# Kernel tuning notes

Measured on AMD Instinct MI355X. Metric: run time of the kernel, lower is better.

The kernel has to match this reference:

```python
import jax, jax.numpy as jnp
import numpy as np

N = 2048      # atoms in one graph
C = 8         # energy_num_channels
CONV = 332.07156


def setup_inputs() -> dict:
    key = jax.random.key(0)
    ks = jax.random.split(key, 12)
    X = jax.random.normal(ks[0], (N, 3), dtype=jnp.float32) * 10.0   # coords (Angstrom-ish)
    embs = jax.random.normal(ks[1], (N, C), dtype=jnp.float32)        # GNN atom embeddings
    qs = jax.random.normal(ks[2], (N,), dtype=jnp.float32) * 0.5      # partial charges
    Ps = jnp.zeros((N, 3), dtype=jnp.float32)                          # dipoles (zeros, as in EnergyNet.forward)
    w0 = jax.random.uniform(ks[3], (N,), dtype=jnp.float32) * 0.5 + 0.1  # vdw_dep
    s0 = jax.random.uniform(ks[4], (N,), dtype=jnp.float32) + 1.0        # vdw_sig
    chainidx = jax.random.randint(ks[5], (N,), 0, 2)
    sf_elec = jax.random.normal(ks[6], (2 * C + 1, 1), dtype=jnp.float32) * 0.1
    sf_elec = sf_elec.at[-1, 0].set(1.0)
    born_factor = jax.random.normal(ks[7], (C,), dtype=jnp.float32) * 0.1 + 1.0
    die_factor = jax.random.normal(ks[8], (C,), dtype=jnp.float32) * 0.1 + 4.0
    depth_factor = jax.random.normal(ks[9], (2 * C, 1), dtype=jnp.float32) * 0.05 + 1.0
    radius_factor = jax.random.normal(ks[10], (2 * C, 1), dtype=jnp.float32) * 0.05 + 1.0
    return dict(X=X, embs=embs, qs=qs, Ps=Ps, w0=w0, s0=s0, chainidx=chainidx,
                sf_elec=sf_elec, born_factor=born_factor, die_factor=die_factor,
                depth_factor=depth_factor, radius_factor=radius_factor)


def _nan_guard(e):
    return jnp.where(jnp.isnan(e), jnp.asarray(1e-6, e.dtype), e)


def _energies(X, embs, qs, Ps, w0, s0, mask, sf_elec, born, die, depth, radius):
    # shared pairwise geometry (original recomputes this in each submodule)
    V = X[None, :, :] - X[:, None, :]               # V[i,j] = X[j]-X[i], [N,N,3]
    D = jnp.sqrt(jnp.sum(V * V + 1e-6, axis=-1))    # [N,N]
    Vp = V + 1e-6
    Vn = Vp / jnp.maximum(jnp.linalg.norm(Vp, axis=-1, keepdims=True), 1e-12)
    invD = 1.0 / (D + 1e-6)

    # ---- Electrostatics ----
    f = sf_elec[:, 0]
    # screening = emb_j . f[:C] + emb_i . f[C:2C] + invD * f[2C]  (decomposed matmul)
    sf = (embs @ f[:C])[None, :] + (embs @ f[C:2 * C])[:, None] + invD * f[2 * C]
    OqP = jnp.einsum('ijk,ik->ij', Vn, Ps)
    OPP = Ps @ Ps.T
    Q12 = jnp.outer(qs, qs)
    invD3 = invD * invD * invD
    E_qq = Q12 * invD * sf
    E_qP = OqP * invD * invD3
    E_PP = OPP * invD3 * invD3
    E_elec = 0.5 * jnp.sum(CONV * mask * (E_qq + E_qP + E_PP))
    E_elec = _nan_guard(E_elec)

    # ---- Solvation (calc_pair=False => only Born self term) ----
    atomic_die = embs @ die + 1e-6
    R = embs @ born + 1.0
    E_self = -(1.0 - 1.0 / atomic_die) * qs / (R + 1e-6)
    E_solv = CONV * jnp.sum(E_self) * 0.01
    E_solv = _nan_guard(E_solv)

    # ---- vdW ----
    rf = radius[:, 0]
    df = depth[:, 0]
    sig_r = jax.nn.sigmoid((embs @ rf[:C])[None, :] + (embs @ rf[C:])[:, None])
    # NB: original broadcasting makes s0_ij = 2*s0[j] (column-only), reproduced faithfully
    s = (2.0 * s0)[None, :] * (0.8 * sig_r + 0.4)
    repl = 5.0 * jnp.exp(-0.3 * D * D * D) * mask
    Dm = D - s
    attr = (jnp.exp(-(Dm - 0.3) ** 2) + jnp.exp(-3.0 * Dm * Dm)
            + jnp.exp(-10.0 * Dm * Dm)) / 3.0 * mask
    w0j = jnp.sqrt(w0 * w0 + 1e-6)[None, :]        # original w0_ij also column-only
    sig_d = jax.nn.sigmoid((embs @ df[:C])[None, :] + (embs @ df[C:])[:, None])
    w = w0j * (sig_d + 0.5)
    E_vdw = jnp.sum(-w * attr + repl)
    E_vdw = _nan_guard(E_vdw)

    return E_vdw, E_elec, E_solv


def reference(X, embs, qs, Ps, w0, s0, chainidx, sf_elec, born_factor, die_factor,
              depth_factor, radius_factor):
    mask = (chainidx[None, :] != chainidx[:, None]).astype(X.dtype)
    return _energies(X, embs, qs, Ps, w0, s0, mask,
                     sf_elec, born_factor, die_factor, depth_factor, radius_factor)
```

## Files before the change

### kernel.cpp

```cpp
#include <hip/hip_runtime.h>

#define NA 2048
#define CDIM 8
#define CONVF 332.07156f
#define PTI 8
#define PTHREADS 512
#define CH 1024
#define PAIR_GRID 258


__global__ __launch_bounds__(256) void pre_kernel(
    const float* __restrict__ X,
    const float* __restrict__ embs,
    const float* __restrict__ qs,
    const float* __restrict__ Ps,
    const float* __restrict__ w0,
    const float* __restrict__ s0,
    const int* __restrict__ chain,
    const float* __restrict__ sf_elec,
    const float* __restrict__ born,
    const float* __restrict__ die,
    const float* __restrict__ depth,
    const float* __restrict__ radius,
    int* __restrict__ wsi,
    float* __restrict__ wsf,
    float4* __restrict__ g0, float4* __restrict__ g1,
    float4* __restrict__ g2, float4* __restrict__ g3,
    float* __restrict__ d_out)
{
    const int b = blockIdx.x, t = threadIdx.x;
    if (b == 8) {
        if (t < 2) d_out[t] = 0.0f;
        return;
    }
    const int i = b * 256 + t;

    const int4 f0 = ((const int4*)chain)[2 * t];
    const int4 f1 = ((const int4*)chain)[2 * t + 1];
    const int s = (f0.x == 0) + (f0.y == 0) + (f0.z == 0) + (f0.w == 0) +
                  (f1.x == 0) + (f1.y == 0) + (f1.z == 0) + (f1.w == 0);
    const int lane = t & 63, wv = t >> 6;
    int x = s;
#pragma unroll
    for (int off = 1; off < 64; off <<= 1) {
        int y = __shfl_up(x, off);
        if (lane >= off) x += y;
    }
    __shared__ int wtot[4];
    __shared__ int gpre[256];
    __shared__ float fsum[4];
    if (lane == 63) wtot[wv] = x;
    __syncthreads();
    int wbase = 0, tot = 0;
#pragma unroll
    for (int k = 0; k < 4; ++k) {
        int v = wtot[k];
        if (k < wv) wbase += v;
        tot += v;
    }
    gpre[t] = wbase + x - s;
    __syncthreads();

    const int g = i >> 3;
    int base = gpre[g];
    for (int a = (g << 3); a < i; ++a) base += (chain[a] == 0);
    const int flag = (chain[i] == 0);
    const int slot = flag ? base : tot + (i - base);

    float e[CDIM];
#pragma unroll
    for (int k = 0; k < CDIM; ++k) e[k] = embs[i * CDIM + k];
    float sfA = 0.f, sfB = 0.f, rfA = 0.f, rfB = 0.f, dfA = 0.f, dfB = 0.f;
    float dieV = 0.f, Rv = 0.f;
#pragma unroll
    for (int k = 0; k < CDIM; ++k) {
        sfA  += e[k] * sf_elec[k];
        sfB  += e[k] * sf_elec[CDIM + k];
        rfA  += e[k] * radius[k];
        rfB  += e[k] * radius[CDIM + k];
        dfA  += e[k] * depth[k];
        dfB  += e[k] * depth[CDIM + k];
        dieV += e[k] * die[k];
        Rv   += e[k] * born[k];
    }
    dieV += 1e-6f;
    Rv += 1.0f;
    const float q = qs[i];
    float es = -(1.0f - 1.0f / dieV) * q / (Rv + 1e-6f);

    const float erA = __expf(-rfA), edA = __expf(-dfA);
    const float erB = __expf(-rfB), edB = __expf(-dfB);
    const float w0j = sqrtf(w0[i] * w0[i] + 1e-6f);

    g0[slot] = make_float4(X[i * 3 + 0], X[i * 3 + 1], X[i * 3 + 2], q);
    g1[slot] = make_float4(sfA, erA, edA, w0j);
    g2[slot] = make_float4(2.0f * s0[i], Ps[i * 3 + 0], Ps[i * 3 + 1], Ps[i * 3 + 2]);
    g3[slot] = make_float4(sfB, erB, edB, 0.0f);

#pragma unroll
    for (int off = 32; off > 0; off >>= 1) es += __shfl_down(es, off);
    if (lane == 0) fsum[wv] = es;
    __syncthreads();
    if (t == 0) {
        wsf[b] = fsum[0] + fsum[1] + fsum[2] + fsum[3];
        if (b == 0) wsi[0] = tot;
    }
}

__global__ __launch_bounds__(512) void pair_kernel(
    const int* __restrict__ cnt,
    const float4* __restrict__ g0, const float4* __restrict__ g1,
    const float4* __restrict__ g2, const float4* __restrict__ g3,
    const float* __restrict__ sf_elec,
    const float* __restrict__ wsf,
    float* __restrict__ d_out)
{
    const int b = blockIdx.x, tid = threadIdx.x;

    if (b == PAIR_GRID - 1) {
        if (tid == 0) {
            float tt = 0.f;
#pragma unroll
            for (int k = 0; k < 8; ++k) tt += wsf[k];
            d_out[2] = CONVF * 0.01f * tt;
        }
        return;
    }

    const int n0 = cnt[0];
    const int B0 = (n0 + PTI - 1) / PTI;
    const int n1 = NA - n0;
    const int B1 = (n1 + PTI - 1) / PTI;
    if (b >= B0 + B1) return;

    int rbase, rend, jbeg, jend;
    if (b < B0) { rbase = b * PTI;             rend = n0; jbeg = n0; jend = NA; }
    else        { rbase = n0 + (b - B0) * PTI; rend = NA; jbeg = 0;  jend = n0; }

    const float f16 = sf_elec[2 * CDIM];

    __shared__ float4 sa[CH];
    __shared__ float4 sb[CH];
    __shared__ float  sc[CH];
    __shared__ float4 sps[PTI];
    __shared__ float se[8], sv[8];

    float xi[PTI], yi[PTI], zi[PTI], qi[PTI], sfB[PTI], erB[PTI], edB[PTI], val[PTI];
    bool hasPs = false;
#pragma unroll
    for (int t = 0; t < PTI; ++t) {
        int r = rbase + t;
        val[t] = (r < rend) ? 1.0f : 0.0f;
        r = max(min(r, rend - 1), 0);
        const float4 p0 = g0[r], p3 = g3[r], p2 = g2[r];
        xi[t] = p0.x; yi[t] = p0.y; zi[t] = p0.z; qi[t] = p0.w;
        sfB[t] = p3.x; erB[t] = p3.y; edB[t] = p3.z;
        hasPs = hasPs || (p2.y != 0.0f) || (p2.z != 0.0f) || (p2.w != 0.0f);
        if (tid == 0) sps[t] = p2;
    }

    float acc_e[PTI], acc_v[PTI];
#pragma unroll
    for (int t = 0; t < PTI; ++t) { acc_e[t] = 0.f; acc_v[t] = 0.f; }

    const float* g2f = (const float*)g2;

    for (int jc = jbeg; jc < jend; jc += CH) {
        const int nc = min(CH, jend - jc);
        __syncthreads();
        for (int k = tid; k < nc; k += PTHREADS) {
            sa[k] = g0[jc + k];
            sb[k] = g1[jc + k];
            sc[k] = g2f[4 * (jc + k)];
        }
        __syncthreads();

        if (!hasPs) {
            for (int jo = tid; jo < nc; jo += PTHREADS) {
                const float4 A = sa[jo];
                const float4 B = sb[jo];
                const float  S = sc[jo];
#pragma unroll
                for (int t = 0; t < PTI; ++t) {
                    const float dx = A.x - xi[t], dy = A.y - yi[t], dz = A.z - zi[t];
                    const float d2 = dx * dx + dy * dy + dz * dz + 3e-6f;
                    const float D = sqrtf(d2);
                    const float invD = __builtin_amdgcn_rcpf(D + 1e-6f);

                    const float sf = B.x + sfB[t] + invD * f16;
                    acc_e[t] += qi[t] * A.w * invD * sf;

                    const float sig_r = __builtin_amdgcn_rcpf(fmaf(B.y, erB[t], 1.0f));
                    const float s = S * fmaf(0.8f, sig_r, 0.4f);
                    const float Dm = D - s;
                    const float Dm2 = Dm * Dm;
                    const float t1 = __expf(-Dm2);
                    const float ta = t1 * __expf(fmaf(0.6f, Dm, -0.09f));
                    const float t2 = t1 * t1;
                    const float t3 = t2 * t1;
                    const float t4 = t2 * t2;
                    const float t8 = t4 * t4;
                    const float t10 = t8 * t2;
                    const float attr = ta + t3 + t10;
                    const float sig_d = __builtin_amdgcn_rcpf(fmaf(B.z, edB[t], 1.0f));
                    const float w = B.w * (sig_d + 0.5f);
                    const float repl = 5.0f * __expf(-0.3f * D * d2);
                    acc_v[t] += repl - w * attr * (1.0f / 3.0f);
                }
            }
        } else {
            for (int jo = tid; jo < nc; jo += PTHREADS) {
                const float4 A = sa[jo];
                const float4 B = sb[jo];
                const float  S = sc[jo];
                const float4 Pj = g2[jc + jo];
#pragma unroll
                for (int t = 0; t < PTI; ++t) {
                    const float dx = A.x - xi[t], dy = A.y - yi[t], dz = A.z - zi[t];
                    const float d2 = dx * dx + dy * dy + dz * dz + 3e-6f;
                    const float D = sqrtf(d2);
                    const float invD = __builtin_amdgcn_rcpf(D + 1e-6f);

                    const float sf = B.x + sfB[t] + invD * f16;
                    float ee = qi[t] * A.w * invD * sf;
                    const float4 Pi = sps[t];
                    const float vpx = dx + 1e-6f, vpy = dy + 1e-6f, vpz = dz + 1e-6f;
                    float vn = sqrtf(vpx * vpx + vpy * vpy + vpz * vpz);
                    vn = fmaxf(vn, 1e-12f);
                    const float OqP = (vpx * Pi.y + vpy * Pi.z + vpz * Pi.w) *
                                      __builtin_amdgcn_rcpf(vn);
                    const float OPP = Pi.y * Pj.y + Pi.z * Pj.z + Pi.w * Pj.w;
                    const float invD2 = invD * invD;
                    const float invD4 = invD2 * invD2;
                    const float invD6 = invD4 * invD2;
                    ee += OqP * invD4 + OPP * invD6;
                    acc_e[t] += ee;

                    const float sig_r = __builtin_amdgcn_rcpf(fmaf(B.y, erB[t], 1.0f));
                    const float s = S * fmaf(0.8f, sig_r, 0.4f);
                    const float Dm = D - s;
                    const float Dm2 = Dm * Dm;
                    const float t1 = __expf(-Dm2);
                    const float ta = t1 * __expf(fmaf(0.6f, Dm, -0.09f));
                    const float t2 = t1 * t1;
                    const float t3 = t2 * t1;
                    const float t4 = t2 * t2;
                    const float t8 = t4 * t4;
                    const float t10 = t8 * t2;
                    const float attr = ta + t3 + t10;
                    const float sig_d = __builtin_amdgcn_rcpf(fmaf(B.z, edB[t], 1.0f));
                    const float w = B.w * (sig_d + 0.5f);
                    const float repl = 5.0f * __expf(-0.3f * D * d2);
                    acc_v[t] += repl - w * attr * (1.0f / 3.0f);
                }
            }
        }
    }

    float ae = 0.f, av = 0.f;
#pragma unroll
    for (int t = 0; t < PTI; ++t) {
        ae += val[t] * acc_e[t];
        av += val[t] * acc_v[t];
    }
#pragma unroll
    for (int off = 32; off > 0; off >>= 1) {
        ae += __shfl_down(ae, off);
        av += __shfl_down(av, off);
    }
    const int lane = tid & 63, wid = tid >> 6;
    if (lane == 0) { se[wid] = ae; sv[wid] = av; }
    __syncthreads();
    if (tid == 0) {
        float te = 0.f, tv = 0.f;
#pragma unroll
        for (int k = 0; k < 8; ++k) { te += se[k]; tv += sv[k]; }
        atomicAdd(d_out + 1, 0.5f * CONVF * te);
        atomicAdd(d_out + 0, tv);
    }
}

extern "C" void kernel_launch(void* const* d_in, const int* in_sizes, int n_in,
                              void* d_out, int out_size, void* d_ws, size_t ws_size,
                              hipStream_t stream) {
    const float* X       = (const float*)d_in[0];
    const float* embs    = (const float*)d_in[1];
    const float* qs      = (const float*)d_in[2];
    const float* Ps      = (const float*)d_in[3];
    const float* w0      = (const float*)d_in[4];
    const float* s0      = (const float*)d_in[5];
    const int*   chain   = (const int*)d_in[6];
    const float* sf_elec = (const float*)d_in[7];
    const float* born    = (const float*)d_in[8];
    const float* die     = (const float*)d_in[9];
    const float* depth   = (const float*)d_in[10];
    const float* radius  = (const float*)d_in[11];
    float* out = (float*)d_out;

    int*   wsi = (int*)d_ws;
    float* wsf = (float*)((char*)d_ws + 64);
    float4* g0 = (float4*)((char*)d_ws + 128);
    float4* g1 = g0 + NA;
    float4* g2 = g1 + NA;
    float4* g3 = g2 + NA;

    pre_kernel<<<9, 256, 0, stream>>>(
        X, embs, qs, Ps, w0, s0, chain, sf_elec, born, die, depth, radius,
        wsi, wsf, g0, g1, g2, g3, out);
    pair_kernel<<<PAIR_GRID, PTHREADS, 0, stream>>>(
        wsi, g0, g1, g2, g3, sf_elec, wsf, out);
}
```

Before: 93.11 us.

## Fuse preprocessing into pair kernel with per-block redundant chain partition

Merges the preprocessing kernel and the pair kernel into a single kernel. Each of the 256 blocks recomputes the chain-sorted per-atom features for all 2048 atoms directly into shared memory, so the workspace round trip and the second launch go away. The output is zeroed with a memset instead. In exchange every block redoes the full embedding projections and exps, and uses a large LDS footprint (about 80KB), which may limit occupancy. Blocks whose rows straddle the chain boundary fall back to a masked loop over all 2048 columns.

```diff
diff --git a/kernel.cpp b/kernel.cpp
--- a/kernel.cpp
+++ b/kernel.cpp
@@ -3,13 +3,12 @@
 #define NA 2048
 #define CDIM 8
 #define CONVF 332.07156f
-#define PTI 8
-#define PTHREADS 512
-#define CH 1024
-#define PAIR_GRID 258
-
-
-__global__ __launch_bounds__(256) void pre_kernel(
+#define BROWS 8
+#define THREADS 512
+#define APT 4
+#define GRID (NA / BROWS)
+
+__global__ __launch_bounds__(THREADS) void fused_kernel(
     const float* __restrict__ X,
     const float* __restrict__ embs,
     const float* __restrict__ qs,
@@ -22,256 +21,234 @@
     const float* __restrict__ die,
     const float* __restrict__ depth,
     const float* __restrict__ radius,
-    int* __restrict__ wsi,
-    float* __restrict__ wsf,
-    float4* __restrict__ g0, float4* __restrict__ g1,
-    float4* __restrict__ g2, float4* __restrict__ g3,
     float* __restrict__ d_out)
 {
     const int b = blockIdx.x, t = threadIdx.x;
-    if (b == 8) {
-        if (t < 2) d_out[t] = 0.0f;
-        return;
-    }
-    const int i = b * 256 + t;
-
-    const int4 f0 = ((const int4*)chain)[2 * t];
-    const int4 f1 = ((const int4*)chain)[2 * t + 1];
-    const int s = (f0.x == 0) + (f0.y == 0) + (f0.z == 0) + (f0.w == 0) +
-                  (f1.x == 0) + (f1.y == 0) + (f1.z == 0) + (f1.w == 0);
     const int lane = t & 63, wv = t >> 6;
-    int x = s;
+
+    __shared__ float4 sa[NA];
+    __shared__ float4 sb[NA];
+    __shared__ float  ssc[NA];
+    __shared__ int    sinv[NA];
+    __shared__ int    wtot[8];
+    __shared__ float  fsum[8];
+    __shared__ float4 srowB[BROWS];
+    __shared__ float4 sps[BROWS];
+    __shared__ float  se[8], sv[8];
+
+    const int ib = APT * t;
+    const int4 cf = ((const int4*)chain)[t];
+    const int f0 = (cf.x == 0), f1 = (cf.y == 0), f2 = (cf.z == 0), f3 = (cf.w == 0);
+    const int cnt = f0 + f1 + f2 + f3;
+    int x = cnt;
 #pragma unroll
     for (int off = 1; off < 64; off <<= 1) {
         int y = __shfl_up(x, off);
         if (lane >= off) x += y;
     }
-    __shared__ int wtot[4];
-    __shared__ int gpre[256];
-    __shared__ float fsum[4];
     if (lane == 63) wtot[wv] = x;
     __syncthreads();
-    int wbase = 0, tot = 0;
-#pragma unroll
-    for (int k = 0; k < 4; ++k) {
+    int wbase = 0, n0 = 0;
+#pragma unroll
+    for (int k = 0; k < 8; ++k) {
         int v = wtot[k];
         if (k < wv) wbase += v;
-        tot += v;
-    }
-    gpre[t] = wbase + x - s;
-    __syncthreads();
-
-    const int g = i >> 3;
-    int base = gpre[g];
-    for (int a = (g << 3); a < i; ++a) base += (chain[a] == 0);
-    const int flag = (chain[i] == 0);
-    const int slot = flag ? base : tot + (i - base);
-
-    float e[CDIM];
-#pragma unroll
-    for (int k = 0; k < CDIM; ++k) e[k] = embs[i * CDIM + k];
-    float sfA = 0.f, sfB = 0.f, rfA = 0.f, rfB = 0.f, dfA = 0.f, dfB = 0.f;
-    float dieV = 0.f, Rv = 0.f;
+        n0 += v;
+    }
+    int run = wbase + x - cnt;
+
+    float fa[CDIM], fr[CDIM], fd[CDIM], fe[CDIM], fb[CDIM];
 #pragma unroll
     for (int k = 0; k < CDIM; ++k) {
-        sfA  += e[k] * sf_elec[k];
-        sfB  += e[k] * sf_elec[CDIM + k];
-        rfA  += e[k] * radius[k];
-        rfB  += e[k] * radius[CDIM + k];
-        dfA  += e[k] * depth[k];
-        dfB  += e[k] * depth[CDIM + k];
-        dieV += e[k] * die[k];
-        Rv   += e[k] * born[k];
-    }
-    dieV += 1e-6f;
-    Rv += 1.0f;
-    const float q = qs[i];
-    float es = -(1.0f - 1.0f / dieV) * q / (Rv + 1e-6f);
-
-    const float erA = __expf(-rfA), edA = __expf(-dfA);
-    const float erB = __expf(-rfB), edB = __expf(-dfB);
-    const float w0j = sqrtf(w0[i] * w0[i] + 1e-6f);
-
-    g0[slot] = make_float4(X[i * 3 + 0], X[i * 3 + 1], X[i * 3 + 2], q);
-    g1[slot] = make_float4(sfA, erA, edA, w0j);
-    g2[slot] = make_float4(2.0f * s0[i], Ps[i * 3 + 0], Ps[i * 3 + 1], Ps[i * 3 + 2]);
-    g3[slot] = make_float4(sfB, erB, edB, 0.0f);
-
+        fa[k] = sf_elec[k];
+        fr[k] = radius[k];
+        fd[k] = depth[k];
+        fe[k] = die[k];
+        fb[k] = born[k];
+    }
+    const float f16 = sf_elec[2 * CDIM];
+
+    float es = 0.0f;
+#pragma unroll
+    for (int h = 0; h < APT; ++h) {
+        const int i = ib + h;
+        const int fh = (h == 0 ? f0 : h == 1 ? f1 : h == 2 ? f2 : f3);
+        const int sl = fh ? run : n0 + (i - run);
+        run += fh;
+
+        float e[CDIM];
+#pragma unroll
+        for (int k = 0; k < CDIM; ++k) e[k] = embs[i * CDIM + k];
+        float sfA = 0.f, rfA = 0.f, dfA = 0.f, dieV = 0.f, Rv = 0.f;
+#pragma unroll
+        for (int k = 0; k < CDIM; ++k) {
+            sfA  += e[k] * fa[k];
+            rfA  += e[k] * fr[k];
+            dfA  += e[k] * fd[k];
+            dieV += e[k] * fe[k];
+            Rv   += e[k] * fb[k];
+        }
+        dieV += 1e-6f;
+        Rv += 1.0f;
+        const float q = qs[i];
+        es += -(1.0f - 1.0f / dieV) * q / (Rv + 1e-6f);
+
+        const float w0v = w0[i];
+        sa[sl]  = make_float4(X[i * 3 + 0], X[i * 3 + 1], X[i * 3 + 2], q);
+        sb[sl]  = make_float4(sfA, __expf(-rfA), __expf(-dfA),
+                              sqrtf(w0v * w0v + 1e-6f));
+        ssc[sl] = 2.0f * s0[i];
+        sinv[sl] = i;
+    }
 #pragma unroll
     for (int off = 32; off > 0; off >>= 1) es += __shfl_down(es, off);
     if (lane == 0) fsum[wv] = es;
     __syncthreads();
-    if (t == 0) {
-        wsf[b] = fsum[0] + fsum[1] + fsum[2] + fsum[3];
-        if (b == 0) wsi[0] = tot;
-    }
-}
-
-__global__ __launch_bounds__(512) void pair_kernel(
-    const int* __restrict__ cnt,
-    const float4* __restrict__ g0, const float4* __restrict__ g1,
-    const float4* __restrict__ g2, const float4* __restrict__ g3,
-    const float* __restrict__ sf_elec,
-    const float* __restrict__ wsf,
-    float* __restrict__ d_out)
-{
-    const int b = blockIdx.x, tid = threadIdx.x;
-
-    if (b == PAIR_GRID - 1) {
-        if (tid == 0) {
-            float tt = 0.f;
-#pragma unroll
-            for (int k = 0; k < 8; ++k) tt += wsf[k];
-            d_out[2] = CONVF * 0.01f * tt;
-        }
-        return;
-    }
-
-    const int n0 = cnt[0];
-    const int B0 = (n0 + PTI - 1) / PTI;
-    const int n1 = NA - n0;
-    const int B1 = (n1 + PTI - 1) / PTI;
-    if (b >= B0 + B1) return;
-
-    int rbase, rend, jbeg, jend;
-    if (b < B0) { rbase = b * PTI;             rend = n0; jbeg = n0; jend = NA; }
-    else        { rbase = n0 + (b - B0) * PTI; rend = NA; jbeg = 0;  jend = n0; }
-
-    const float f16 = sf_elec[2 * CDIM];
-
-    __shared__ float4 sa[CH];
-    __shared__ float4 sb[CH];
-    __shared__ float  sc[CH];
-    __shared__ float4 sps[PTI];
-    __shared__ float se[8], sv[8];
-
-    float xi[PTI], yi[PTI], zi[PTI], qi[PTI], sfB[PTI], erB[PTI], edB[PTI], val[PTI];
-    bool hasPs = false;
-#pragma unroll
-    for (int t = 0; t < PTI; ++t) {
-        int r = rbase + t;
-        val[t] = (r < rend) ? 1.0f : 0.0f;
-        r = max(min(r, rend - 1), 0);
-        const float4 p0 = g0[r], p3 = g3[r], p2 = g2[r];
-        xi[t] = p0.x; yi[t] = p0.y; zi[t] = p0.z; qi[t] = p0.w;
-        sfB[t] = p3.x; erB[t] = p3.y; edB[t] = p3.z;
-        hasPs = hasPs || (p2.y != 0.0f) || (p2.z != 0.0f) || (p2.w != 0.0f);
-        if (tid == 0) sps[t] = p2;
-    }
-
-    float acc_e[PTI], acc_v[PTI];
-#pragma unroll
-    for (int t = 0; t < PTI; ++t) { acc_e[t] = 0.f; acc_v[t] = 0.f; }
-
-    const float* g2f = (const float*)g2;
-
-    for (int jc = jbeg; jc < jend; jc += CH) {
-        const int nc = min(CH, jend - jc);
-        __syncthreads();
-        for (int k = tid; k < nc; k += PTHREADS) {
-            sa[k] = g0[jc + k];
-            sb[k] = g1[jc + k];
-            sc[k] = g2f[4 * (jc + k)];
-        }
-        __syncthreads();
-
-        if (!hasPs) {
-            for (int jo = tid; jo < nc; jo += PTHREADS) {
-                const float4 A = sa[jo];
-                const float4 B = sb[jo];
-                const float  S = sc[jo];
-#pragma unroll
-                for (int t = 0; t < PTI; ++t) {
-                    const float dx = A.x - xi[t], dy = A.y - yi[t], dz = A.z - zi[t];
-                    const float d2 = dx * dx + dy * dy + dz * dz + 3e-6f;
-                    const float D = sqrtf(d2);
-                    const float invD = __builtin_amdgcn_rcpf(D + 1e-6f);
-
-                    const float sf = B.x + sfB[t] + invD * f16;
-                    acc_e[t] += qi[t] * A.w * invD * sf;
-
-                    const float sig_r = __builtin_amdgcn_rcpf(fmaf(B.y, erB[t], 1.0f));
-                    const float s = S * fmaf(0.8f, sig_r, 0.4f);
-                    const float Dm = D - s;
-                    const float Dm2 = Dm * Dm;
-                    const float t1 = __expf(-Dm2);
-                    const float ta = t1 * __expf(fmaf(0.6f, Dm, -0.09f));
-                    const float t2 = t1 * t1;
-                    const float t3 = t2 * t1;
-                    const float t4 = t2 * t2;
-                    const float t8 = t4 * t4;
-                    const float t10 = t8 * t2;
-                    const float attr = ta + t3 + t10;
-                    const float sig_d = __builtin_amdgcn_rcpf(fmaf(B.z, edB[t], 1.0f));
-                    const float w = B.w * (sig_d + 0.5f);
-                    const float repl = 5.0f * __expf(-0.3f * D * d2);
-                    acc_v[t] += repl - w * attr * (1.0f / 3.0f);
-                }
+
+    const int rbase = b * BROWS;
+    if (t < BROWS) {
+        const int orig = sinv[rbase + t];
+        float e[CDIM];
+#pragma unroll
+        for (int k = 0; k < CDIM; ++k) e[k] = embs[orig * CDIM + k];
+        float sfB = 0.f, rfB = 0.f, dfB = 0.f;
+#pragma unroll
+        for (int k = 0; k < CDIM; ++k) {
+            sfB += e[k] * sf_elec[CDIM + k];
+            rfB += e[k] * radius[CDIM + k];
+            dfB += e[k] * depth[CDIM + k];
+        }
+        srowB[t] = make_float4(sfB, __expf(-rfB), __expf(-dfB), 0.0f);
+        sps[t]   = make_float4(0.0f, Ps[orig * 3 + 0], Ps[orig * 3 + 1],
+                               Ps[orig * 3 + 2]);
+    }
+    if (b == 0 && t == 0) {
+        float tt = 0.f;
+#pragma unroll
+        for (int k = 0; k < 8; ++k) tt += fsum[k];
+        d_out[2] = CONVF * 0.01f * tt;
+    }
+    __syncthreads();
+
+    float xi[BROWS], yi[BROWS], zi[BROWS], qi[BROWS];
+    float sfB[BROWS], erB[BROWS], edB[BROWS];
+    bool anyPs = false;
+#pragma unroll
+    for (int rt = 0; rt < BROWS; ++rt) {
+        const float4 p  = sa[rbase + rt];
+        const float4 rb = srowB[rt];
+        const float4 pp = sps[rt];
+        xi[rt] = p.x; yi[rt] = p.y; zi[rt] = p.z; qi[rt] = p.w;
+        sfB[rt] = rb.x; erB[rt] = rb.y; edB[rt] = rb.z;
+        anyPs = anyPs || (pp.y != 0.f) || (pp.z != 0.f) || (pp.w != 0.f);
+    }
+    const bool uniform = (rbase >= n0) || (rbase + BROWS <= n0);
+
+    float acc_e[BROWS], acc_v[BROWS];
+#pragma unroll
+    for (int rt = 0; rt < BROWS; ++rt) { acc_e[rt] = 0.f; acc_v[rt] = 0.f; }
+
+    if (uniform && !anyPs) {
+        const bool r0 = (rbase < n0);
+        const int jbeg = r0 ? n0 : 0;
+        const int jend = r0 ? NA : n0;
+        for (int j = jbeg + t; j < jend; j += THREADS) {
+            const float4 A = sa[j];
+            const float4 B = sb[j];
+            const float  S = ssc[j];
+#pragma unroll
+            for (int rt = 0; rt < BROWS; ++rt) {
+                const float dx = A.x - xi[rt], dy = A.y - yi[rt], dz = A.z - zi[rt];
+                const float d2 = dx * dx + dy * dy + dz * dz + 3e-6f;
+                const float D = sqrtf(d2);
+                const float invD = __builtin_amdgcn_rcpf(D + 1e-6f);
+
+                const float sf = B.x + sfB[rt] + invD * f16;
+                acc_e[rt] += qi[rt] * A.w * invD * sf;
+
+                const float sig_r = __builtin_amdgcn_rcpf(fmaf(B.y, erB[rt], 1.0f));
+                const float s = S * fmaf(0.8f, sig_r, 0.4f);
+                const float Dm = D - s;
+                const float t1 = __expf(-Dm * Dm);
+                const float ta = t1 * __expf(fmaf(0.6f, Dm, -0.09f));
+                const float t2 = t1 * t1;
+                const float t3 = t2 * t1;
+                const float t4 = t2 * t2;
+                const float t8 = t4 * t4;
+                const float t10 = t8 * t2;
+                const float attr = ta + t3 + t10;
+                const float sig_d = __builtin_amdgcn_rcpf(fmaf(B.z, edB[rt], 1.0f));
+                const float w = B.w * (sig_d + 0.5f);
+                const float repl = 5.0f * __expf(-0.3f * D * d2);
+                acc_v[rt] += repl - w * attr * (1.0f / 3.0f);
             }
-        } else {
-            for (int jo = tid; jo < nc; jo += PTHREADS) {
-                const float4 A = sa[jo];
-                const float4 B = sb[jo];
-                const float  S = sc[jo];
-                const float4 Pj = g2[jc + jo];
-#pragma unroll
-                for (int t = 0; t < PTI; ++t) {
-                    const float dx = A.x - xi[t], dy = A.y - yi[t], dz = A.z - zi[t];
-                    const float d2 = dx * dx + dy * dy + dz * dz + 3e-6f;
-                    const float D = sqrtf(d2);
-                    const float invD = __builtin_amdgcn_rcpf(D + 1e-6f);
-
-                    const float sf = B.x + sfB[t] + invD * f16;
-                    float ee = qi[t] * A.w * invD * sf;
-                    const float4 Pi = sps[t];
+        }
+    } else {
+        for (int j = t; j < NA; j += THREADS) {
+            const float4 A = sa[j];
+            const float4 B = sb[j];
+            const float  S = ssc[j];
+            const bool j0 = (j < n0);
+            float pjx = 0.f, pjy = 0.f, pjz = 0.f;
+            if (anyPs) {
+                const int oj = sinv[j];
+                pjx = Ps[oj * 3 + 0]; pjy = Ps[oj * 3 + 1]; pjz = Ps[oj * 3 + 2];
+            }
+#pragma unroll
+            for (int rt = 0; rt < BROWS; ++rt) {
+                const float m = (((rbase + rt) < n0) != j0) ? 1.0f : 0.0f;
+                const float dx = A.x - xi[rt], dy = A.y - yi[rt], dz = A.z - zi[rt];
+                const float d2 = dx * dx + dy * dy + dz * dz + 3e-6f;
+                const float D = sqrtf(d2);
+                const float invD = __builtin_amdgcn_rcpf(D + 1e-6f);
+
+                const float sf = B.x + sfB[rt] + invD * f16;
+                float ee = qi[rt] * A.w * invD * sf;
+                if (anyPs) {
+                    const float4 Pi = sps[rt];
                     const float vpx = dx + 1e-6f, vpy = dy + 1e-6f, vpz = dz + 1e-6f;
                     float vn = sqrtf(vpx * vpx + vpy * vpy + vpz * vpz);
                     vn = fmaxf(vn, 1e-12f);
                     const float OqP = (vpx * Pi.y + vpy * Pi.z + vpz * Pi.w) *
                                       __builtin_amdgcn_rcpf(vn);
-                    const float OPP = Pi.y * Pj.y + Pi.z * Pj.z + Pi.w * Pj.w;
+                    const float OPP = Pi.y * pjx + Pi.z * pjy + Pi.w * pjz;
                     const float invD2 = invD * invD;
                     const float invD4 = invD2 * invD2;
                     const float invD6 = invD4 * invD2;
                     ee += OqP * invD4 + OPP * invD6;
-                    acc_e[t] += ee;
-
-                    const float sig_r = __builtin_amdgcn_rcpf(fmaf(B.y, erB[t], 1.0f));
-                    const float s = S * fmaf(0.8f, sig_r, 0.4f);
-                    const float Dm = D - s;
-                    const float Dm2 = Dm * Dm;
-                    const float t1 = __expf(-Dm2);
-                    const float ta = t1 * __expf(fmaf(0.6f, Dm, -0.09f));
-                    const float t2 = t1 * t1;
-                    const float t3 = t2 * t1;
-                    const float t4 = t2 * t2;
-                    const float t8 = t4 * t4;
-                    const float t10 = t8 * t2;
-                    const float attr = ta + t3 + t10;
-                    const float sig_d = __builtin_amdgcn_rcpf(fmaf(B.z, edB[t], 1.0f));
-                    const float w = B.w * (sig_d + 0.5f);
-                    const float repl = 5.0f * __expf(-0.3f * D * d2);
-                    acc_v[t] += repl - w * attr * (1.0f / 3.0f);
                 }
+                acc_e[rt] += m * ee;
+
+                const float sig_r = __builtin_amdgcn_rcpf(fmaf(B.y, erB[rt], 1.0f));
+                const float s = S * fmaf(0.8f, sig_r, 0.4f);
+                const float Dm = D - s;
+                const float t1 = __expf(-Dm * Dm);
+                const float ta = t1 * __expf(fmaf(0.6f, Dm, -0.09f));
+                const float t2 = t1 * t1;
+                const float t3 = t2 * t1;
+                const float t4 = t2 * t2;
+                const float t8 = t4 * t4;
+                const float t10 = t8 * t2;
+                const float attr = ta + t3 + t10;
+                const float sig_d = __builtin_amdgcn_rcpf(fmaf(B.z, edB[rt], 1.0f));
+                const float w = B.w * (sig_d + 0.5f);
+                const float repl = 5.0f * __expf(-0.3f * D * d2);
+                acc_v[rt] += m * (repl - w * attr * (1.0f / 3.0f));
             }
         }
     }
 
     float ae = 0.f, av = 0.f;
 #pragma unroll
-    for (int t = 0; t < PTI; ++t) {
-        ae += val[t] * acc_e[t];
-        av += val[t] * acc_v[t];
-    }
+    for (int rt = 0; rt < BROWS; ++rt) { ae += acc_e[rt]; av += acc_v[rt]; }
 #pragma unroll
     for (int off = 32; off > 0; off >>= 1) {
         ae += __shfl_down(ae, off);
         av += __shfl_down(av, off);
     }
-    const int lane = tid & 63, wid = tid >> 6;
-    if (lane == 0) { se[wid] = ae; sv[wid] = av; }
-    __syncthreads();
-    if (tid == 0) {
+    if (lane == 0) { se[wv] = ae; sv[wv] = av; }
+    __syncthreads();
+    if (t == 0) {
         float te = 0.f, tv = 0.f;
 #pragma unroll
         for (int k = 0; k < 8; ++k) { te += se[k]; tv += sv[k]; }
@@ -297,16 +274,7 @@
     const float* radius  = (const float*)d_in[11];
     float* out = (float*)d_out;
 
-    int*   wsi = (int*)d_ws;
-    float* wsf = (float*)((char*)d_ws + 64);
-    float4* g0 = (float4*)((char*)d_ws + 128);
-    float4* g1 = g0 + NA;
-    float4* g2 = g1 + NA;
-    float4* g3 = g2 + NA;
-
-    pre_kernel<<<9, 256, 0, stream>>>(
-        X, embs, qs, Ps, w0, s0, chain, sf_elec, born, die, depth, radius,
-        wsi, wsf, g0, g1, g2, g3, out);
-    pair_kernel<<<PAIR_GRID, PTHREADS, 0, stream>>>(
-        wsi, g0, g1, g2, g3, sf_elec, wsf, out);
+    hipMemsetAsync(d_out, 0, 3 * sizeof(float), stream);
+    fused_kernel<<<GRID, THREADS, 0, stream>>>(
+        X, embs, qs, Ps, w0, s0, chain, sf_elec, born, die, depth, radius, out);
 }
```

Measured after the change: 93.14 us. About the same (+0.0%).
